# Kernel optimization log

Hardware: AMD Instinct MI355X
Metric: run time of the kernel (lower is better)

The kernel has to match this reference:

```python
import jax, jax.numpy as jnp
import numpy as np

BSZ, SEQ, D, H, E = 4, 2048, 128, 4, 65536
C = D  # out_channels per head (GATConv out_channels=embed_dim)


def setup_inputs() -> dict:
    key = jax.random.key(0)
    ks = jax.random.split(key, 10)
    s = jax.random.normal(ks[0], (BSZ, SEQ, D), dtype=jnp.float32)
    # edge_index with src != dst (GATConv removes self loops then re-adds them)
    src = jax.random.randint(ks[1], (E,), 0, SEQ)
    dst = (src + 1 + jax.random.randint(ks[2], (E,), 0, SEQ - 1)) % SEQ
    edge_index = jnp.stack([src, dst]).astype(jnp.int32)  # [2, E]
    glorot = lambda k, shp, fan: (jax.random.normal(k, shp, jnp.float32) * np.float32(np.sqrt(2.0 / fan)))
    W = glorot(ks[3], (H * C, D), D + H * C)        # gat_conv.lin weight
    att_src = glorot(ks[4], (H, C), C)               # gat_conv.att_src
    att_dst = glorot(ks[5], (H, C), C)               # gat_conv.att_dst
    bias = jnp.zeros((H * C,), jnp.float32)          # gat_conv.bias (concat=True)
    Wo = glorot(ks[6], (D, H * C), H * C + D)        # out_proj weight
    bo = jnp.zeros((D,), jnp.float32)
    return {"s": s, "edge_index": edge_index, "W": W, "att_src": att_src,
            "att_dst": att_dst, "bias": bias, "Wo": Wo, "bo": bo}


def reference(s, edge_index, W, att_src, att_dst, bias, Wo, bo):
    bsz, L, D_ = s.shape
    H_, C_ = att_src.shape
    N = bsz * L
    # shared source/target linear transform: [N, H, C]
    x = (s.reshape(N, D_) @ W.T).reshape(N, H_, C_)
    # batch the edge list: tile edges bsz times with per-graph node offsets
    offsets = jnp.arange(bsz, dtype=edge_index.dtype) * L
    ei = (edge_index[:, None, :] + offsets[None, :, None]).reshape(2, -1)
    # add self loops for every node (input has none)
    loops = jnp.arange(N, dtype=edge_index.dtype)
    src = jnp.concatenate([ei[0], loops])
    dst = jnp.concatenate([ei[1], loops])
    # per-node attention terms: [N, H]
    a_src = jnp.einsum('nhc,hc->nh', x, att_src)
    a_dst = jnp.einsum('nhc,hc->nh', x, att_dst)
    # per-edge logits, LeakyReLU(0.2): [Etot, H]
    logits = jax.nn.leaky_relu(a_src[src] + a_dst[dst], negative_slope=0.2)
    # segment softmax over incoming edges of each dst node
    m = jax.ops.segment_max(logits, dst, num_segments=N)
    e = jnp.exp(logits - m[dst])
    denom = jax.ops.segment_sum(e, dst, num_segments=N)
    alpha = e / denom[dst]                                   # [Etot, H]
    # weighted scatter-aggregate: [N, H, C]
    out = jax.ops.segment_sum(alpha[:, :, None] * x[src], dst, num_segments=N)
    out = out.reshape(N, H_ * C_) + bias                     # concat heads + bias
    proj = out @ Wo.T + bo                                   # out_proj
    return proj.reshape(bsz, L, -1)
```

## Files before the change

kernel.cpp:

```cpp
#include <hip/hip_runtime.h>

constexpr int BSZ = 4, SEQ = 2048, D = 128, H = 4, E = 65536;
constexpr int N  = BSZ * SEQ;
constexpr int HC = H * D;
constexpr int SLOTS = 128;
constexpr int MAXE  = SLOTS + 4;

typedef __attribute__((ext_vector_type(8))) short s16x8;
typedef __attribute__((ext_vector_type(4))) float f32x4;

__device__ inline unsigned short f2bf(float v) {
    unsigned u = __float_as_uint(v);
    return (unsigned short)((u + 0x7fffu + ((u >> 16) & 1u)) >> 16);
}
__device__ inline float bf2f(unsigned short h) { return __uint_as_float(((unsigned)h) << 16); }

__global__ __launch_bounds__(256) void prep_all(const float* __restrict__ W,
                                                const float* __restrict__ att_src,
                                                const float* __restrict__ att_dst,
                                                const float* __restrict__ bias,
                                                const float* __restrict__ Wo,
                                                const float* __restrict__ bo,
                                                float* __restrict__ w_src,
                                                float* __restrict__ w_dst,
                                                unsigned short* __restrict__ p_hi,
                                                unsigned short* __restrict__ p_lo,
                                                float* __restrict__ cvec,
                                                int* __restrict__ cursor) {
    __shared__ float part[4];
    const int b = blockIdx.x, tid = threadIdx.x;
    if (b < 256) {
        int h = b & 3;
        int d = (b >> 2) * 2 + (tid >> 7);
        int k = tid & 127;
        float acc = 0.f;
        for (int c = 0; c < D; ++c)
            acc += Wo[d * HC + h * D + c] * W[(h * D + c) * D + k];
        unsigned short hi = f2bf(acc);
        int ct = d >> 4, lrow = d & 15;
        int kg = h * D + k, kstep = kg >> 5, kin = kg & 31;
        size_t idx = ((size_t)(ct * 16 + kstep) * 64 + (kin >> 3) * 16 + lrow) * 8 + (kin & 7);
        p_hi[idx] = hi;
        p_lo[idx] = f2bf(acc - bf2f(hi));
    } else if (b < 384) {
        int d = b - 256;
        float a = bias[tid] * Wo[d * HC + tid] + bias[tid + 256] * Wo[d * HC + tid + 256];
        #pragma unroll
        for (int off = 32; off; off >>= 1) a += __shfl_xor(a, off);
        if ((tid & 63) == 0) part[tid >> 6] = a;
        __syncthreads();
        if (tid == 0) cvec[d] = part[0] + part[1] + part[2] + part[3] + bo[d];
    } else if (b < 386) {
        int t = (b - 384) * 256 + tid;
        int h = t >> 7, dd = t & 127;
        float ws = 0.f, wd = 0.f;
        for (int c = 0; c < D; ++c) {
            float wv = W[(h * D + c) * D + dd];
            ws += att_src[h * D + c] * wv;
            wd += att_dst[h * D + c] * wv;
        }
        w_src[t] = ws;
        w_dst[t] = wd;
    } else {
        int idx = (b - 386) * 256 + tid;
        if (idx < SEQ) cursor[idx] = 0;
    }
}

__global__ __launch_bounds__(256) void att_fill(const float* __restrict__ s,
                                                const float* __restrict__ w_src,
                                                const float* __restrict__ w_dst,
                                                const int* __restrict__ ei,
                                                float* __restrict__ a_src,
                                                float* __restrict__ a_dst,
                                                int* __restrict__ cursor,
                                                int* __restrict__ csr0) {
    const int bid = blockIdx.x, tid = threadIdx.x;
    if (bid < 256) {
        int e = bid * 256 + tid;
        int src = ei[e], dst = ei[E + e];
        int slot = atomicAdd(&cursor[dst], 1);
        if (slot < SLOTS) csr0[dst * SLOTS + slot] = src;
    }
    const int wave = tid >> 6, lane = tid & 63;
    const int n = bid * 4 + wave;
    float s0 = s[n * D + lane];
    float s1 = s[n * D + 64 + lane];
    #pragma unroll
    for (int h = 0; h < H; ++h) {
        float ps = s0 * w_src[h * D + lane] + s1 * w_src[h * D + 64 + lane];
        float pd = s0 * w_dst[h * D + lane] + s1 * w_dst[h * D + 64 + lane];
        #pragma unroll
        for (int off = 32; off; off >>= 1) {
            ps += __shfl_xor(ps, off);
            pd += __shfl_xor(pd, off);
        }
        if (lane == 0) {
            a_src[n * H + h] = ps;
            a_dst[n * H + h] = pd;
        }
    }
}

__global__ __launch_bounds__(512, 4) void agg_out(const int* __restrict__ cursor,
                                                  const int* __restrict__ csr0,
                                                  const float* __restrict__ a_src,
                                                  const float* __restrict__ a_dst,
                                                  const float* __restrict__ s,
                                                  const unsigned short* __restrict__ p_hi,
                                                  const unsigned short* __restrict__ p_lo,
                                                  const float* __restrict__ cvec,
                                                  float* __restrict__ out) {
    __shared__ short    zf[2][16][512];
    __shared__ float    sh_alpha[8][MAXE][4];
    __shared__ int      sh_src[8][MAXE];
    const int bid = blockIdx.x;
    const int batch = (bid & 7) >> 1;
    const int itile = ((bid >> 3) << 1) | (bid & 1);
    const int tile  = batch * 128 + itile;
    const int w = threadIdx.x >> 6, lane = threadIdx.x & 63;
    const int half = lane >> 5, l32 = lane & 31;

    for (int rep = 0; rep < 2; ++rep) {
        const int r = w * 2 + rep;
        const int n = tile * 16 + r;
        const int dloc = n & 2047;
        int deg = cursor[dloc];
        deg = (deg < SLOTS) ? deg : SLOTS;
        const int beg = dloc * SLOTS;
        const int cnt = deg + 1;
        float4 adv = *reinterpret_cast<const float4*>(&a_dst[n * H]);
        float ad[4] = {adv.x, adv.y, adv.z, adv.w};
        float mx[4] = {-1e30f, -1e30f, -1e30f, -1e30f};
        for (int i = lane; i < cnt; i += 64) {
            int sg = (i < deg) ? (csr0[beg + i] + (batch << 11)) : n;
            sh_src[w][i] = sg;
            float4 asv = *reinterpret_cast<const float4*>(&a_src[sg * H]);
            float lg[4] = {asv.x, asv.y, asv.z, asv.w};
            #pragma unroll
            for (int h = 0; h < 4; ++h) {
                float l = lg[h] + ad[h];
                l = (l > 0.f) ? l : 0.2f * l;
                sh_alpha[w][i][h] = l;
                mx[h] = fmaxf(mx[h], l);
            }
        }
        #pragma unroll
        for (int h = 0; h < 4; ++h)
            #pragma unroll
            for (int off = 32; off; off >>= 1) mx[h] = fmaxf(mx[h], __shfl_xor(mx[h], off));
        float sm[4] = {0.f, 0.f, 0.f, 0.f};
        for (int i = lane; i < cnt; i += 64) {
            #pragma unroll
            for (int h = 0; h < 4; ++h) {
                float ev = __expf(sh_alpha[w][i][h] - mx[h]);
                sh_alpha[w][i][h] = ev;
                sm[h] += ev;
            }
        }
        #pragma unroll
        for (int h = 0; h < 4; ++h)
            #pragma unroll
            for (int off = 32; off; off >>= 1) sm[h] += __shfl_xor(sm[h], off);
        float inv[4];
        #pragma unroll
        for (int h = 0; h < 4; ++h) inv[h] = 1.f / sm[h];

        const int coff = l32 * 4;
        float acc[4][4] = {};
        int i = 0;
        for (; i + 8 <= cnt; i += 8) {
            int i0 = i + half, i1 = i + 2 + half, i2 = i + 4 + half, i3 = i + 6 + half;
            int sg0 = sh_src[w][i0], sg1 = sh_src[w][i1];
            int sg2 = sh_src[w][i2], sg3 = sh_src[w][i3];
            float4 sv0 = *reinterpret_cast<const float4*>(&s[(size_t)sg0 * D + coff]);
            float4 sv1 = *reinterpret_cast<const float4*>(&s[(size_t)sg1 * D + coff]);
            float4 sv2 = *reinterpret_cast<const float4*>(&s[(size_t)sg2 * D + coff]);
            float4 sv3 = *reinterpret_cast<const float4*>(&s[(size_t)sg3 * D + coff]);
            float4 a0 = *reinterpret_cast<const float4*>(&sh_alpha[w][i0][0]);
            float4 a1 = *reinterpret_cast<const float4*>(&sh_alpha[w][i1][0]);
            float4 a2 = *reinterpret_cast<const float4*>(&sh_alpha[w][i2][0]);
            float4 a3 = *reinterpret_cast<const float4*>(&sh_alpha[w][i3][0]);
            float al0[4] = {a0.x, a0.y, a0.z, a0.w};
            float al1[4] = {a1.x, a1.y, a1.z, a1.w};
            float al2[4] = {a2.x, a2.y, a2.z, a2.w};
            float al3[4] = {a3.x, a3.y, a3.z, a3.w};
            float c0[4] = {sv0.x, sv0.y, sv0.z, sv0.w};
            float c1[4] = {sv1.x, sv1.y, sv1.z, sv1.w};
            float c2[4] = {sv2.x, sv2.y, sv2.z, sv2.w};
            float c3[4] = {sv3.x, sv3.y, sv3.z, sv3.w};
            #pragma unroll
            for (int h = 0; h < 4; ++h)
                #pragma unroll
                for (int c = 0; c < 4; ++c)
                    acc[h][c] += al0[h] * c0[c] + al1[h] * c1[c]
                               + al2[h] * c2[c] + al3[h] * c3[c];
        }
        for (; i < cnt; i += 2) {
            int ii = i + half;
            if (ii < cnt) {
                int sg = sh_src[w][ii];
                float4 sv = *reinterpret_cast<const float4*>(&s[(size_t)sg * D + coff]);
                float4 alv = *reinterpret_cast<const float4*>(&sh_alpha[w][ii][0]);
                float al[4] = {alv.x, alv.y, alv.z, alv.w};
                float cv[4] = {sv.x, sv.y, sv.z, sv.w};
                #pragma unroll
                for (int h = 0; h < 4; ++h)
                    #pragma unroll
                    for (int c = 0; c < 4; ++c) acc[h][c] += al[h] * cv[c];
            }
        }
        #pragma unroll
        for (int h = 0; h < 4; ++h)
            #pragma unroll
            for (int c = 0; c < 4; ++c) acc[h][c] += __shfl_xor(acc[h][c], 32);
        #pragma unroll
        for (int hh = 0; hh < 2; ++hh) {
            int h = half * 2 + hh;
            ushort4 zh, zl;
            float v0 = acc[h][0] * inv[h], v1 = acc[h][1] * inv[h];
            float v2 = acc[h][2] * inv[h], v3 = acc[h][3] * inv[h];
            zh.x = f2bf(v0); zh.y = f2bf(v1); zh.z = f2bf(v2); zh.w = f2bf(v3);
            zl.x = f2bf(v0 - bf2f(zh.x)); zl.y = f2bf(v1 - bf2f(zh.y));
            zl.z = f2bf(v2 - bf2f(zh.z)); zl.w = f2bf(v3 - bf2f(zh.w));
            const int kstep = h * 4 + (l32 >> 3);
            const int slot  = (l32 >> 1) & 3;
            const int jo    = (l32 & 1) * 4;
            const int off   = (slot * 16 + r) * 8 + jo;
            *reinterpret_cast<ushort4*>(&zf[0][kstep][off]) = zh;
            *reinterpret_cast<ushort4*>(&zf[1][kstep][off]) = zl;
        }
    }
    __syncthreads();

    f32x4 acc = {0.f, 0.f, 0.f, 0.f};
    const unsigned short* pb = p_hi + ((size_t)w * 16 * 64 + lane) * 8;
    const unsigned short* pl = p_lo + ((size_t)w * 16 * 64 + lane) * 8;
    #pragma unroll
    for (int ks = 0; ks < 16; ++ks) {
        s16x8 ah = *reinterpret_cast<const s16x8*>(&zf[0][ks][lane * 8]);
        s16x8 al = *reinterpret_cast<const s16x8*>(&zf[1][ks][lane * 8]);
        s16x8 bh = *reinterpret_cast<const s16x8*>(pb + ks * 512);
        s16x8 bl = *reinterpret_cast<const s16x8*>(pl + ks * 512);
        acc = __builtin_amdgcn_mfma_f32_16x16x32_bf16(ah, bh, acc, 0, 0, 0);
        acc = __builtin_amdgcn_mfma_f32_16x16x32_bf16(ah, bl, acc, 0, 0, 0);
        acc = __builtin_amdgcn_mfma_f32_16x16x32_bf16(al, bh, acc, 0, 0, 0);
    }
    const int ocol = w * 16 + (lane & 15);
    const int orow = tile * 16 + (lane >> 4) * 4;
    const float cb = cvec[ocol];
    #pragma unroll
    for (int r2 = 0; r2 < 4; ++r2)
        out[(size_t)(orow + r2) * D + ocol] = acc[r2] + cb;
}

extern "C" void kernel_launch(void* const* d_in, const int* in_sizes, int n_in,
                              void* d_out, int out_size, void* d_ws, size_t ws_size,
                              hipStream_t stream) {
    const float* s       = (const float*)d_in[0];
    const int*   ei      = (const int*)d_in[1];
    const float* W       = (const float*)d_in[2];
    const float* att_src = (const float*)d_in[3];
    const float* att_dst = (const float*)d_in[4];
    const float* bias    = (const float*)d_in[5];
    const float* Wo      = (const float*)d_in[6];
    const float* bo      = (const float*)d_in[7];
    float* out = (float*)d_out;

    char* ws = (char*)d_ws;
    float* w_src = (float*)ws; ws += 512 * 4;
    float* w_dst = (float*)ws; ws += 512 * 4;
    float* a_src = (float*)ws; ws += (size_t)N * H * 4;
    float* a_dst = (float*)ws; ws += (size_t)N * H * 4;
    float* cvec  = (float*)ws; ws += 512;
    unsigned short* p_hi = (unsigned short*)ws; ws += (size_t)D * HC * 2;
    unsigned short* p_lo = (unsigned short*)ws; ws += (size_t)D * HC * 2;
    int* cursor = (int*)ws; ws += SEQ * 4;
    int* csr0   = (int*)ws; ws += (size_t)SEQ * SLOTS * 4;

    prep_all<<<394, 256, 0, stream>>>(W, att_src, att_dst, bias, Wo, bo,
                                      w_src, w_dst, p_hi, p_lo, cvec, cursor);
    att_fill<<<N / 4, 256, 0, stream>>>(s, w_src, w_dst, ei, a_src, a_dst, cursor, csr0);
    agg_out<<<N / 16, 512, 0, stream>>>(cursor, csr0, a_src, a_dst, s,
                                        p_hi, p_lo, cvec, out);
}
```

Before: 47.31 us.

## Batch both rows' softmax in registers and prefetch projection weights before barrier

The per-row loop is split into phases. Both destination rows first issue their CSR index and a_src gathers together, then compute the softmax fully in registers (two edges per lane), then aggregate. This removes the strided loops and the extra shared-memory round trips for the logits, and lets the dependent global loads of both rows overlap. The first MFMA B-operand and bias loads are hoisted above the __syncthreads. In exchange the degree cap drops from SLOTS to SLOTS-1 so a row fits in 128 slots, which could drop an edge for very high in-degree nodes, and register pressure rises.

```diff
diff --git a/kernel.cpp b/kernel.cpp
--- a/kernel.cpp
+++ b/kernel.cpp
@@ -4,7 +4,6 @@
 constexpr int N  = BSZ * SEQ;
 constexpr int HC = H * D;
 constexpr int SLOTS = 128;
-constexpr int MAXE  = SLOTS + 4;
 
 typedef __attribute__((ext_vector_type(8))) short s16x8;
 typedef __attribute__((ext_vector_type(4))) float f32x4;
@@ -112,8 +111,8 @@
                                                   const float* __restrict__ cvec,
                                                   float* __restrict__ out) {
     __shared__ short    zf[2][16][512];
-    __shared__ float    sh_alpha[8][MAXE][4];
-    __shared__ int      sh_src[8][MAXE];
+    __shared__ float    sh_alpha[8][2][SLOTS][4];
+    __shared__ int      sh_src[8][2][SLOTS];
     const int bid = blockIdx.x;
     const int batch = (bid & 7) >> 1;
     const int itile = ((bid >> 3) << 1) | (bid & 1);
@@ -121,66 +120,85 @@
     const int w = threadIdx.x >> 6, lane = threadIdx.x & 63;
     const int half = lane >> 5, l32 = lane & 31;
 
+    int    cnts[2];
+    float4 asa[2], asb[2], adv[2];
+    bool   vA[2], vB[2];
+    #pragma unroll
     for (int rep = 0; rep < 2; ++rep) {
         const int r = w * 2 + rep;
         const int n = tile * 16 + r;
         const int dloc = n & 2047;
         int deg = cursor[dloc];
-        deg = (deg < SLOTS) ? deg : SLOTS;
+        deg = (deg < SLOTS - 1) ? deg : (SLOTS - 1);
         const int beg = dloc * SLOTS;
         const int cnt = deg + 1;
-        float4 adv = *reinterpret_cast<const float4*>(&a_dst[n * H]);
-        float ad[4] = {adv.x, adv.y, adv.z, adv.w};
-        float mx[4] = {-1e30f, -1e30f, -1e30f, -1e30f};
-        for (int i = lane; i < cnt; i += 64) {
-            int sg = (i < deg) ? (csr0[beg + i] + (batch << 11)) : n;
-            sh_src[w][i] = sg;
-            float4 asv = *reinterpret_cast<const float4*>(&a_src[sg * H]);
-            float lg[4] = {asv.x, asv.y, asv.z, asv.w};
-            #pragma unroll
-            for (int h = 0; h < 4; ++h) {
-                float l = lg[h] + ad[h];
-                l = (l > 0.f) ? l : 0.2f * l;
-                sh_alpha[w][i][h] = l;
-                mx[h] = fmaxf(mx[h], l);
-            }
+        cnts[rep] = cnt;
+        adv[rep] = *reinterpret_cast<const float4*>(&a_dst[n * H]);
+        const int ia = lane, ib = lane + 64;
+        int sa = (ia < deg) ? (csr0[beg + ia] + (batch << 11)) : n;
+        int sb = (ib < deg) ? (csr0[beg + ib] + (batch << 11)) : n;
+        vA[rep] = (ia < cnt);
+        vB[rep] = (ib < cnt);
+        asa[rep] = *reinterpret_cast<const float4*>(&a_src[sa * H]);
+        asb[rep] = *reinterpret_cast<const float4*>(&a_src[sb * H]);
+        sh_src[w][rep][ia] = sa;
+        sh_src[w][rep][ib] = sb;
+    }
+    float invs[2][4];
+    #pragma unroll
+    for (int rep = 0; rep < 2; ++rep) {
+        float ad[4] = {adv[rep].x, adv[rep].y, adv[rep].z, adv[rep].w};
+        float la[4] = {asa[rep].x, asa[rep].y, asa[rep].z, asa[rep].w};
+        float lb[4] = {asb[rep].x, asb[rep].y, asb[rep].z, asb[rep].w};
+        float mx[4];
+        #pragma unroll
+        for (int h = 0; h < 4; ++h) {
+            float x = la[h] + ad[h];
+            la[h] = vA[rep] ? ((x > 0.f) ? x : 0.2f * x) : -1e30f;
+            float y = lb[h] + ad[h];
+            lb[h] = vB[rep] ? ((y > 0.f) ? y : 0.2f * y) : -1e30f;
+            mx[h] = fmaxf(la[h], lb[h]);
         }
         #pragma unroll
         for (int h = 0; h < 4; ++h)
             #pragma unroll
             for (int off = 32; off; off >>= 1) mx[h] = fmaxf(mx[h], __shfl_xor(mx[h], off));
-        float sm[4] = {0.f, 0.f, 0.f, 0.f};
-        for (int i = lane; i < cnt; i += 64) {
-            #pragma unroll
-            for (int h = 0; h < 4; ++h) {
-                float ev = __expf(sh_alpha[w][i][h] - mx[h]);
-                sh_alpha[w][i][h] = ev;
-                sm[h] += ev;
-            }
-        }
+        float e0[4], e1[4], sm[4];
+        #pragma unroll
+        for (int h = 0; h < 4; ++h) {
+            e0[h] = vA[rep] ? __expf(la[h] - mx[h]) : 0.f;
+            e1[h] = vB[rep] ? __expf(lb[h] - mx[h]) : 0.f;
+            sm[h] = e0[h] + e1[h];
+        }
+        *reinterpret_cast<float4*>(&sh_alpha[w][rep][lane][0])      = make_float4(e0[0], e0[1], e0[2], e0[3]);
+        *reinterpret_cast<float4*>(&sh_alpha[w][rep][lane + 64][0]) = make_float4(e1[0], e1[1], e1[2], e1[3]);
         #pragma unroll
         for (int h = 0; h < 4; ++h)
             #pragma unroll
             for (int off = 32; off; off >>= 1) sm[h] += __shfl_xor(sm[h], off);
-        float inv[4];
-        #pragma unroll
-        for (int h = 0; h < 4; ++h) inv[h] = 1.f / sm[h];
-
+        #pragma unroll
+        for (int h = 0; h < 4; ++h) invs[rep][h] = 1.f / sm[h];
+    }
+
+    #pragma unroll
+    for (int rep = 0; rep < 2; ++rep) {
+        const int r = w * 2 + rep;
+        const int cnt = cnts[rep];
         const int coff = l32 * 4;
         float acc[4][4] = {};
         int i = 0;
         for (; i + 8 <= cnt; i += 8) {
             int i0 = i + half, i1 = i + 2 + half, i2 = i + 4 + half, i3 = i + 6 + half;
-            int sg0 = sh_src[w][i0], sg1 = sh_src[w][i1];
-            int sg2 = sh_src[w][i2], sg3 = sh_src[w][i3];
+            int sg0 = sh_src[w][rep][i0], sg1 = sh_src[w][rep][i1];
+            int sg2 = sh_src[w][rep][i2], sg3 = sh_src[w][rep][i3];
             float4 sv0 = *reinterpret_cast<const float4*>(&s[(size_t)sg0 * D + coff]);
             float4 sv1 = *reinterpret_cast<const float4*>(&s[(size_t)sg1 * D + coff]);
             float4 sv2 = *reinterpret_cast<const float4*>(&s[(size_t)sg2 * D + coff]);
             float4 sv3 = *reinterpret_cast<const float4*>(&s[(size_t)sg3 * D + coff]);
-            float4 a0 = *reinterpret_cast<const float4*>(&sh_alpha[w][i0][0]);
-            float4 a1 = *reinterpret_cast<const float4*>(&sh_alpha[w][i1][0]);
-            float4 a2 = *reinterpret_cast<const float4*>(&sh_alpha[w][i2][0]);
-            float4 a3 = *reinterpret_cast<const float4*>(&sh_alpha[w][i3][0]);
+            float4 a0 = *reinterpret_cast<const float4*>(&sh_alpha[w][rep][i0][0]);
+            float4 a1 = *reinterpret_cast<const float4*>(&sh_alpha[w][rep][i1][0]);
+            float4 a2 = *reinterpret_cast<const float4*>(&sh_alpha[w][rep][i2][0]);
+            float4 a3 = *reinterpret_cast<const float4*>(&sh_alpha[w][rep][i3][0]);
             float al0[4] = {a0.x, a0.y, a0.z, a0.w};
             float al1[4] = {a1.x, a1.y, a1.z, a1.w};
             float al2[4] = {a2.x, a2.y, a2.z, a2.w};
@@ -199,9 +217,9 @@
         for (; i < cnt; i += 2) {
             int ii = i + half;
             if (ii < cnt) {
-                int sg = sh_src[w][ii];
+                int sg = sh_src[w][rep][ii];
                 float4 sv = *reinterpret_cast<const float4*>(&s[(size_t)sg * D + coff]);
-                float4 alv = *reinterpret_cast<const float4*>(&sh_alpha[w][ii][0]);
+                float4 alv = *reinterpret_cast<const float4*>(&sh_alpha[w][rep][ii][0]);
                 float al[4] = {alv.x, alv.y, alv.z, alv.w};
                 float cv[4] = {sv.x, sv.y, sv.z, sv.w};
                 #pragma unroll
@@ -218,8 +236,8 @@
         for (int hh = 0; hh < 2; ++hh) {
             int h = half * 2 + hh;
             ushort4 zh, zl;
-            float v0 = acc[h][0] * inv[h], v1 = acc[h][1] * inv[h];
-            float v2 = acc[h][2] * inv[h], v3 = acc[h][3] * inv[h];
+            float v0 = acc[h][0] * invs[rep][h], v1 = acc[h][1] * invs[rep][h];
+            float v2 = acc[h][2] * invs[rep][h], v3 = acc[h][3] * invs[rep][h];
             zh.x = f2bf(v0); zh.y = f2bf(v1); zh.z = f2bf(v2); zh.w = f2bf(v3);
             zl.x = f2bf(v0 - bf2f(zh.x)); zl.y = f2bf(v1 - bf2f(zh.y));
             zl.z = f2bf(v2 - bf2f(zh.z)); zl.w = f2bf(v3 - bf2f(zh.w));
@@ -231,13 +249,24 @@
             *reinterpret_cast<ushort4*>(&zf[1][kstep][off]) = zl;
         }
     }
-    __syncthreads();
-
-    f32x4 acc = {0.f, 0.f, 0.f, 0.f};
     const unsigned short* pb = p_hi + ((size_t)w * 16 * 64 + lane) * 8;
     const unsigned short* pl = p_lo + ((size_t)w * 16 * 64 + lane) * 8;
-    #pragma unroll
-    for (int ks = 0; ks < 16; ++ks) {
+    s16x8 bh0 = *reinterpret_cast<const s16x8*>(pb);
+    s16x8 bl0 = *reinterpret_cast<const s16x8*>(pl);
+    const int ocol = w * 16 + (lane & 15);
+    const float cb = cvec[ocol];
+    __syncthreads();
+
+    f32x4 acc = {0.f, 0.f, 0.f, 0.f};
+    {
+        s16x8 ah = *reinterpret_cast<const s16x8*>(&zf[0][0][lane * 8]);
+        s16x8 al = *reinterpret_cast<const s16x8*>(&zf[1][0][lane * 8]);
+        acc = __builtin_amdgcn_mfma_f32_16x16x32_bf16(ah, bh0, acc, 0, 0, 0);
+        acc = __builtin_amdgcn_mfma_f32_16x16x32_bf16(ah, bl0, acc, 0, 0, 0);
+        acc = __builtin_amdgcn_mfma_f32_16x16x32_bf16(al, bh0, acc, 0, 0, 0);
+    }
+    #pragma unroll
+    for (int ks = 1; ks < 16; ++ks) {
         s16x8 ah = *reinterpret_cast<const s16x8*>(&zf[0][ks][lane * 8]);
         s16x8 al = *reinterpret_cast<const s16x8*>(&zf[1][ks][lane * 8]);
         s16x8 bh = *reinterpret_cast<const s16x8*>(pb + ks * 512);
@@ -246,9 +275,7 @@
         acc = __builtin_amdgcn_mfma_f32_16x16x32_bf16(ah, bl, acc, 0, 0, 0);
         acc = __builtin_amdgcn_mfma_f32_16x16x32_bf16(al, bh, acc, 0, 0, 0);
     }
-    const int ocol = w * 16 + (lane & 15);
     const int orow = tile * 16 + (lane >> 4) * 4;
-    const float cb = cvec[ocol];
     #pragma unroll
     for (int r2 = 0; r2 < 4; ++r2)
         out[(size_t)(orow + r2) * D + ocol] = acc[r2] + cb;
```

After: 48.43 us. 2.4% more time.
